# Optimization experiments

Measured on AMD Instinct MI355X. Metric: run time of the kernel, lower is better.

## Reference

```python
import jax, jax.numpy as jnp
import numpy as np

NG, NC = 4096, 4096
FIN_G, FIN_C, D = 512, 512, 256
ALPHA = 0.2
NEG = -9.0e15

def leaky(x):
    return jnp.where(x >= 0, x, ALPHA * x)

def setup_inputs() -> dict:
    key = jax.random.key(0)
    ks = jax.random.split(key, 16)
    gene_x = jax.random.normal(ks[0], (NG, FIN_G), jnp.float32)
    cell_x = jax.random.normal(ks[1], (NC, FIN_C), jnp.float32)
    gene_adj = (jax.random.uniform(ks[2], (NG, NG)) < 0.05).astype(jnp.float32)
    gene_adj = jnp.maximum(gene_adj, jnp.eye(NG, dtype=jnp.float32))
    cell_adj = (jax.random.uniform(ks[3], (NC, NC)) < 0.05).astype(jnp.float32)
    cell_adj = jnp.maximum(cell_adj, jnp.eye(NC, dtype=jnp.float32))
    gene_cell_adj = (jax.random.uniform(ks[4], (NG, NC)) < 0.05).astype(jnp.float32)
    s = 1.414 * np.sqrt(6.0)
    def xav(k, shape):
        lim = s / np.sqrt(shape[0] + shape[1])
        return jax.random.uniform(k, shape, jnp.float32, -lim, lim)
    Wg = xav(ks[5], (D, FIN_G))
    Wc = xav(ks[6], (D, FIN_C))
    a_gg = xav(ks[7], (2 * D, 1))
    a_gc = xav(ks[8], (2 * D, 1))
    a_cc = xav(ks[9], (2 * D, 1))
    a_cg = xav(ks[10], (2 * D, 1))
    gate_g_w = xav(ks[11], (1, D))
    gate_c_w = xav(ks[12], (1, D))
    gate_g_b = jnp.full((1,), -2.0, jnp.float32)
    gate_c_b = jnp.full((1,), -2.0, jnp.float32)
    return dict(gene_x=gene_x, cell_x=cell_x, gene_adj=gene_adj, cell_adj=cell_adj,
                gene_cell_adj=gene_cell_adj, Wg=Wg, Wc=Wc, a_gg=a_gg, a_gc=a_gc,
                a_cc=a_cc, a_cg=a_cg, gate_g_w=gate_g_w, gate_g_b=gate_g_b,
                gate_c_w=gate_c_w, gate_c_b=gate_c_b)

def _gat_block(src_h, dst_h, a, adj):
    # attention of src rows over dst columns; adj: [Ns, Nd]
    d = src_h.shape[1]
    s1 = src_h @ a[:d, :]          # [Ns,1]
    s2 = dst_h @ a[d:, :]          # [Nd,1]
    e = leaky(s1 + s2.T)           # [Ns,Nd]
    att = jax.nn.softmax(jnp.where(adj > 0, e, NEG), axis=1)
    return att @ dst_h             # [Ns,d]

def reference(gene_x, cell_x, gene_adj, cell_adj, gene_cell_adj,
              Wg, Wc, a_gg, a_gc, a_cc, a_cg,
              gate_g_w, gate_g_b, gate_c_w, gate_c_b):
    gene_h = gene_x @ Wg.T   # [Ng,D]
    cell_h = cell_x @ Wc.T   # [Nc,D]
    gene_from_gene = _gat_block(gene_h, gene_h, a_gg, gene_adj)
    gene_from_cell = _gat_block(gene_h, cell_h, a_gc, gene_cell_adj)
    cell_from_cell = _gat_block(cell_h, cell_h, a_cc, cell_adj)
    cell_from_gene = _gat_block(cell_h, gene_h, a_cg, gene_cell_adj.T)
    gamma_g = jax.nn.sigmoid(gene_h @ gate_g_w.T + gate_g_b)  # [Ng,1]
    gamma_c = jax.nn.sigmoid(cell_h @ gate_c_w.T + gate_c_b)  # [Nc,1]
    gene_out = leaky(gene_h + gene_from_gene + gamma_g * gene_from_cell)
    cell_out = leaky(cell_h + cell_from_cell + gamma_c * cell_from_gene)
    return gene_out, cell_out
```

## Files before the change

### kernel.cpp

```cpp
#include <hip/hip_runtime.h>
#include <stdint.h>

#define NGC 4096
#define FIN 512
#define DD  256

typedef __attribute__((ext_vector_type(8))) short short8;
typedef __attribute__((ext_vector_type(4))) float f32x4;
typedef unsigned short u16;
typedef unsigned int   u32;
typedef unsigned long long u64;

static __device__ __forceinline__ float bf2f(u16 u){ return __uint_as_float(((u32)u)<<16); }
static __device__ __forceinline__ u16 f2bf(float f){
  u32 u = __float_as_uint(f);
  u += 0x7fffu + ((u>>16)&1u);
  return (u16)(u>>16);
}
static __device__ __forceinline__ u64 pack4bf(f32x4 v){
  u64 r;
  r  = (u64)f2bf(v[0]);
  r |= (u64)f2bf(v[1]) << 16;
  r |= (u64)f2bf(v[2]) << 32;
  r |= (u64)f2bf(v[3]) << 48;
  return r;
}
static __device__ __forceinline__ float lk(float x){ return fmaxf(x, 0.2f*x); }
static __device__ __forceinline__ u64 shfl_xor64(u64 x, int m){
  u32 lo = (u32)x, hi = (u32)(x >> 32);
  lo = __shfl_xor(lo, m); hi = __shfl_xor(hi, m);
  return ((u64)hi << 32) | lo;
}
static __device__ __forceinline__ u64 spread4(u64 x){
  x &= 0xFFFFull;
  x = (x | (x << 24)) & 0x000000FF000000FFull;
  x = (x | (x << 12)) & 0x000F000F000F000Full;
  x = (x | (x << 6))  & 0x0303030303030303ull;
  x = (x | (x << 3))  & 0x1111111111111111ull;
  return x;
}
static __device__ __forceinline__ void gl16(const void* g, void* l){
  __builtin_amdgcn_global_load_lds(
    (const __attribute__((address_space(1))) void*)g,
    (__attribute__((address_space(3))) void*)l, 16, 0, 0);
}

__global__ __launch_bounds__(512) void k_front(
    const float* __restrict__ gene_adj, const float* __restrict__ cell_adj,
    const float* __restrict__ gc_adj,   u64* __restrict__ packbits,
    const float* __restrict__ xg, const float* __restrict__ xc,
    const float* __restrict__ Wgf, const float* __restrict__ Wcf,
    float* __restrict__ hg, float* __restrict__ hc,
    u16* __restrict__ hTg, u16* __restrict__ hTc)
{
  __shared__ __align__(16) char smem[32768];
  const int t = threadIdx.x;
  const int wid = t >> 6, lane = t & 63;

  if(blockIdx.x < 256){
    int w = blockIdx.x*8 + wid;
    int row0 = w*6;
    const int sel = lane >> 2;
    const int sh = (lane & 3) * 16;

    float4 bufA[16], bufB[16];
    {
      int m = row0 >> 12;
      const float* sp = (m==0) ? gene_adj : (m==1) ? cell_adj : gc_adj;
      const float* rp = sp + (size_t)(row0 & 4095)*NGC + lane*4;
      #pragma unroll
      for(int j=0;j<16;j++) bufA[j] = *(const float4*)(rp + j*256);
    }
    #pragma unroll
    for(int i=0;i<6;i++){
      const bool evn = (i & 1) == 0;
      if(i < 5){
        int row = row0 + i + 1;
        int m = row >> 12;
        const float* sp = (m==0) ? gene_adj : (m==1) ? cell_adj : gc_adj;
        const float* rp = sp + (size_t)(row & 4095)*NGC + lane*4;
        if(evn){
          #pragma unroll
          for(int j=0;j<16;j++) bufB[j] = *(const float4*)(rp + j*256);
        } else {
          #pragma unroll
          for(int j=0;j<16;j++) bufA[j] = *(const float4*)(rp + j*256);
        }
      }
      u64 k0=0, k1=0, k2=0, k3=0;
      #pragma unroll
      for(int j=0;j<16;j++){
        float4 v = evn ? bufA[j] : bufB[j];
        u64 b0 = __ballot(v.x != 0.0f);
        u64 b1 = __ballot(v.y != 0.0f);
        u64 b2 = __ballot(v.z != 0.0f);
        u64 b3 = __ballot(v.w != 0.0f);
        if(sel == j){ k0=b0; k1=b1; k2=b2; k3=b3; }
      }
      u64 wv = spread4(k0 >> sh) | (spread4(k1 >> sh) << 1)
             | (spread4(k2 >> sh) << 2) | (spread4(k3 >> sh) << 3);
      int row = row0 + i;
      packbits[((size_t)(row >> 12) << 18) + (size_t)(row & 4095)*64 + lane] = wv;
    }
    return;
  }

  const int bid = blockIdx.x - 256;
  const int side = bid >> 6;
  const float* x = side ? xc : xg;
  const float* Wf = side ? Wcf : Wgf;
  float* h  = side ? hc : hg;
  u16*  hT  = side ? hTc : hTg;
  const int r0 = (bid & 63) * 64;
  const int lrow = lane & 15, lhi = lane >> 4;

  f32x4 acc[4][2];
  const f32x4 z4 = {0.f,0.f,0.f,0.f};
  #pragma unroll
  for(int i=0;i<4;i++){ acc[i][0]=z4; acc[i][1]=z4; }

  const int r = t >> 3, c8 = t & 7;
  for(int k0 = 0; k0 < FIN; k0 += 64){
    const float* xp = x + (size_t)(r0 + r)*FIN + k0 + c8*8;
    float4 xa = *(const float4*)xp;
    float4 xb = *(const float4*)(xp + 4);
    short8 xv;
    xv[0]=(short)f2bf(xa.x); xv[1]=(short)f2bf(xa.y);
    xv[2]=(short)f2bf(xa.z); xv[3]=(short)f2bf(xa.w);
    xv[4]=(short)f2bf(xb.x); xv[5]=(short)f2bf(xb.y);
    xv[6]=(short)f2bf(xb.z); xv[7]=(short)f2bf(xb.w);
    int wbyte = r*128 + (((c8 ^ (r & 7)) & 7) << 4);
    *(short8*)(smem + wbyte) = xv;
    __syncthreads();
    #pragma unroll
    for(int ksub = 0; ksub < 2; ksub++){
      short8 b[2];
      #pragma unroll
      for(int nf=0; nf<2; nf++){
        int n = wid*32 + nf*16 + lrow;
        const float* wp = Wf + (size_t)n*FIN + k0 + ksub*32 + lhi*8;
        float4 wa = *(const float4*)wp;
        float4 wb = *(const float4*)(wp + 4);
        short8 bb;
        bb[0]=(short)f2bf(wa.x); bb[1]=(short)f2bf(wa.y);
        bb[2]=(short)f2bf(wa.z); bb[3]=(short)f2bf(wa.w);
        bb[4]=(short)f2bf(wb.x); bb[5]=(short)f2bf(wb.y);
        bb[6]=(short)f2bf(wb.z); bb[7]=(short)f2bf(wb.w);
        b[nf] = bb;
      }
      #pragma unroll
      for(int mf=0; mf<4; mf++){
        int row = mf*16 + lrow;
        int g = ksub*4 + lhi;
        short8 a = *(const short8*)(smem + row*128 + (((g ^ (row & 7)) & 7) << 4));
        #pragma unroll
        for(int nf=0; nf<2; nf++)
          acc[mf][nf] = __builtin_amdgcn_mfma_f32_16x16x32_bf16(a, b[nf], acc[mf][nf], 0,0,0);
      }
    }
    __syncthreads();
  }
  #pragma unroll
  for(int mf=0; mf<4; mf++){
    #pragma unroll
    for(int nf=0; nf<2; nf++){
      int col = wid*32 + nf*16 + lrow;
      #pragma unroll
      for(int j=0;j<4;j++){
        int row = mf*16 + lhi*4 + j;
        float v = acc[mf][nf][j];
        h[(size_t)(r0+row)*DD + col] = v;
        int byte_ = col*128 + (((row*2) ^ ((col & 7)<<4)));
        *(u16*)(smem + byte_) = f2bf(v);
      }
    }
  }
  __syncthreads();
  {
    int n = t >> 1, half = t & 1;
    #pragma unroll
    for(int gi=0; gi<4; gi++){
      int g = half*4 + gi;
      int byte_ = n*128 + (((g ^ (n & 7)) & 7) << 4);
      short8 v = *(const short8*)(smem + byte_);
      int kcol = r0 + g*8;
      size_t off = (size_t)(kcol>>5)*8192 + (size_t)(n>>4)*512
                 + ((kcol>>3)&3)*128 + (n&15)*8;
      *(short8*)(hT + off) = v;
    }
  }
}

__global__ __launch_bounds__(256) void k_bitTT(
    const u64* __restrict__ gcb, u64* __restrict__ bT)
{
  int t = threadIdx.x, wid = t>>6, lane = t&63;
  int id = blockIdx.x*4 + wid;
  int G = id & 63, C = id >> 6;

  u64 x = gcb[(size_t)(64*G + lane)*64 + C];

  const u64 M1  = 0xAAAAAAAAAAAAAAAAull;
  const u64 M2  = 0xCCCCCCCCCCCCCCCCull;
  const u64 M4  = 0xF0F0F0F0F0F0F0F0ull;
  const u64 M8  = 0xFF00FF00FF00FF00ull;
  const u64 M16 = 0xFFFF0000FFFF0000ull;
  const u64 M32 = 0xFFFFFFFF00000000ull;
  #define TSTEP(S, M) { u64 y = shfl_xor64(x, S); \
    x = (lane & S) ? ((x & (M)) | ((y >> S) & ~(M))) \
                   : ((x & ~(M)) | ((y << S) & (M))); }
  TSTEP(32, M32) TSTEP(16, M16) TSTEP(8, M8)
  TSTEP(4,  M4)  TSTEP(2,  M2)  TSTEP(1, M1)
  #undef TSTEP

  bT[(size_t)(64*C + lane)*64 + G] = x;
}

__global__ __launch_bounds__(256) void k_svec(
    const float* __restrict__ hg, const float* __restrict__ hc,
    const float* __restrict__ a_gg, const float* __restrict__ a_gc,
    const float* __restrict__ a_cc, const float* __restrict__ a_cg,
    const float* __restrict__ gw_g, const float* __restrict__ gb_g,
    const float* __restrict__ gw_c, const float* __restrict__ gb_c,
    float* __restrict__ sbuf)
{
  int t = threadIdx.x, wid = t>>6, lane = t&63;
  int idx = blockIdx.x * 4 + wid;
  int side = idx >> 12;
  int row  = idx & 4095;
  const float* h = (side ? hc : hg) + (size_t)row*DD;
  const float* v0 = (side ? a_cc : a_gg);
  const float* v1 = (side ? a_cc : a_gg) + DD;
  const float* v2 = (side ? a_cg : a_gc);
  const float* v3 = (side ? a_gc : a_cg) + DD;
  const float* gw = side ? gw_c : gw_g;
  float bias = (side ? gb_c : gb_g)[0];

  float4 hv = *(const float4*)(h + lane*4);
  float4 w0 = *(const float4*)(v0 + lane*4);
  float4 w1 = *(const float4*)(v1 + lane*4);
  float4 w2 = *(const float4*)(v2 + lane*4);
  float4 w3 = *(const float4*)(v3 + lane*4);
  float4 w4 = *(const float4*)(gw + lane*4);

  float d0 = hv.x*w0.x + hv.y*w0.y + hv.z*w0.z + hv.w*w0.w;
  float d1 = hv.x*w1.x + hv.y*w1.y + hv.z*w1.z + hv.w*w1.w;
  float d2 = hv.x*w2.x + hv.y*w2.y + hv.z*w2.z + hv.w*w2.w;
  float d3 = hv.x*w3.x + hv.y*w3.y + hv.z*w3.z + hv.w*w3.w;
  float d4 = hv.x*w4.x + hv.y*w4.y + hv.z*w4.z + hv.w*w4.w;
  #pragma unroll
  for(int s=1;s<64;s<<=1){
    d0 += __shfl_xor(d0, s); d1 += __shfl_xor(d1, s); d2 += __shfl_xor(d2, s);
    d3 += __shfl_xor(d3, s); d4 += __shfl_xor(d4, s);
  }
  if(lane == 0){
    float gam = 1.f/(1.f + __expf(-(d4 + bias)));
    if(side == 0){
      sbuf[0*4096+row]=d0; sbuf[1*4096+row]=d1; sbuf[2*4096+row]=d2;
      sbuf[3*4096+row]=d3; sbuf[4*4096+row]=gam;
    } else {
      sbuf[5*4096+row]=d0; sbuf[6*4096+row]=d1; sbuf[8*4096+row]=d2;
      sbuf[7*4096+row]=d3; sbuf[9*4096+row]=gam;
    }
  }
}

__global__ __launch_bounds__(256,2) void k_gat(
    const float* __restrict__ sbuf,
    const uint8_t* __restrict__ packbits, const uint8_t* __restrict__ bitsT,
    const u16* __restrict__ hTg, const u16* __restrict__ hTc,
    u16* __restrict__ part, float* __restrict__ Zpart)
{
  const int mode = blockIdx.z;
  const int kc   = blockIdx.y;
  const int nodebase = blockIdx.x * 64;
  const int kcbase   = kc * 2048;

  const float* s1; const float* s2; const uint8_t* bits; const u16* hT;
  if(mode == 0){ s1 = sbuf;        s2 = sbuf+4096;   bits = packbits;           hT = hTg; }
  else if(mode == 1){ s1 = sbuf+2*4096; s2 = sbuf+7*4096; bits = packbits+4194304; hT = hTc; }
  else if(mode == 2){ s1 = sbuf+5*4096; s2 = sbuf+6*4096; bits = packbits+2097152; hT = hTc; }
  else { s1 = sbuf+8*4096; s2 = sbuf+3*4096; bits = bitsT; hT = hTg; }

  const int t = threadIdx.x, wid = t>>6, lane = t&63, lrow = lane&15, lhi = lane>>4;
  const int kh = wid >> 1;
  const int ng_sub = wid & 1;

  __shared__ __align__(16) char U[81920];
  char* A_lds  = U;
  char* mask_l = U + 65536;

  {
    int row = t>>2, seg = t&3;
    const char* g = (const char*)bits + (size_t)(nodebase+row)*512 + kc*256 + seg*64;
    char* drow_ = mask_l + row*256;
    #pragma unroll
    for(int i=0;i<4;i++){
      int slot = seg*4 + i;
      *(ulonglong2*)(drow_ + (((slot ^ (row&7)))<<4)) = *(const ulonglong2*)(g + i*16);
    }
  }
  const char* hTb = (const char*)hT;
  {
    const char* g = hTb + ((size_t)kc*64 + kh*32 + 0)*16384 + ng_sub*8192 + lane*16;
    char* l = A_lds + 0*32768 + kh*16384 + ng_sub*8192;
    #pragma unroll
    for(int i=0;i<8;i++) gl16(g + i*1024, l + i*1024);
  }
  float mxv = -1e30f;
  #pragma unroll
  for(int i=0;i<16;i++){
    float4 v = *(const float4*)(s2 + lane*64 + i*4);
    mxv = fmaxf(mxv, fmaxf(fmaxf(v.x,v.y), fmaxf(v.z,v.w)));
  }
  #pragma unroll
  for(int sh=1; sh<64; sh<<=1) mxv = fmaxf(mxv, __shfl_xor(mxv, sh));
  const float maxs2 = mxv;

  const int wnode = nodebase + ng_sub*32;
  const float L2E = 1.4426950408889634f;
  float c1[2], c2[2], z[2];
  #pragma unroll
  for(int nf=0; nf<2; nf++){
    float s1v = s1[wnode + nf*16 + lrow];
    float m = lk(s1v + maxs2);
    c1[nf] = (s1v - m)*L2E;
    c2[nf] = (0.2f*s1v - m)*L2E;
    z[nf] = 0.f;
  }

  f32x4 acc[16][2];
  const f32x4 zz = {0.f,0.f,0.f,0.f};
  #pragma unroll
  for(int i=0;i<16;i++){ acc[i][0]=zz; acc[i][1]=zz; }

  const float* s2g = s2 + kcbase + kh*1024 + lhi*8;
  const char* mrow0 = mask_l + (ng_sub*32 + lrow)*256;
  const char* mrow1 = mask_l + (ng_sub*32 + 16 + lrow)*256;
  const int mx0 = (ng_sub*32 + lrow) & 7, mx1 = (ng_sub*32 + 16 + lrow) & 7;

  float4 csA = *(const float4*)(s2g);
  float4 csB = *(const float4*)(s2g + 4);

  __syncthreads();

  #pragma unroll 1
  for(int s=0; s<32; s++){
    const int cur = s & 1;
    if(s < 31){
      const char* g = hTb + ((size_t)kc*64 + kh*32 + s + 1)*16384 + ng_sub*8192 + lane*16;
      char* l = A_lds + (cur^1)*32768 + kh*16384 + ng_sub*8192;
      #pragma unroll
      for(int i=0;i<8;i++) gl16(g + i*1024, l + i*1024);
    }
    float4 sA = csA, sB = csB;
    if(s < 31){
      csA = *(const float4*)(s2g + (s+1)*32);
      csB = *(const float4*)(s2g + (s+1)*32 + 4);
    }
    float e1[8], e2[8];
    {
      float sv[8] = {sA.x,sA.y,sA.z,sA.w,sB.x,sB.y,sB.z,sB.w};
      #pragma unroll
      for(int j=0;j<8;j++){ e1[j] = sv[j]*L2E; e2[j] = sv[j]*(0.2f*L2E); }
    }
    const int slot = kh*8 + (s>>2), win = (s&3)*4;
    u32 mw0 = *(const u32*)(mrow0 + ((slot ^ mx0)<<4) + win);
    u32 mw1 = *(const u32*)(mrow1 + ((slot ^ mx1)<<4) + win);
    short8 b[2];
    #pragma unroll
    for(int nf=0; nf<2; nf++){
      u32 mw = nf ? mw1 : mw0;
      u32 w4[4];
      #pragma unroll
      for(int pr=0; pr<4; pr++){
        float bit0 = (float)((mw >> (lhi*8 + 2*pr  )) & 1u);
        float bit1 = (float)((mw >> (lhi*8 + 2*pr+1)) & 1u);
        float p0 = __builtin_amdgcn_exp2f(fmaxf(c1[nf]+e1[2*pr  ], c2[nf]+e2[2*pr  ])) * bit0;
        float p1 = __builtin_amdgcn_exp2f(fmaxf(c1[nf]+e1[2*pr+1], c2[nf]+e2[2*pr+1])) * bit1;
        z[nf] += p0 + p1;
        u32 q0 = __float_as_uint(p0) + 0x8000u;
        u32 q1 = __float_as_uint(p1) + 0x8000u;
        w4[pr] = (q1 & 0xFFFF0000u) | (q0 >> 16);
      }
      union{ u32 u[4]; short8 s8; } cv;
      cv.u[0]=w4[0]; cv.u[1]=w4[1]; cv.u[2]=w4[2]; cv.u[3]=w4[3];
      b[nf] = cv.s8;
    }
    const char* Af = A_lds + cur*32768 + kh*16384 + lane*16;
    #pragma unroll
    for(int mf=0; mf<16; mf++){
      short8 a = *(const short8*)(Af + mf*1024);
      acc[mf][0] = __builtin_amdgcn_mfma_f32_16x16x32_bf16(a, b[0], acc[mf][0], 0,0,0);
      acc[mf][1] = __builtin_amdgcn_mfma_f32_16x16x32_bf16(a, b[1], acc[mf][1], 0,0,0);
    }
    __syncthreads();
  }

  #pragma unroll
  for(int nf=0; nf<2; nf++){
    z[nf] += __shfl_xor(z[nf], 16);
    z[nf] += __shfl_xor(z[nf], 32);
  }
  if(lhi == 0){
    float* zp = Zpart + (size_t)(mode*4 + kc*2 + kh)*4096 + wnode;
    zp[lrow]      = z[0];
    zp[16 + lrow] = z[1];
  }

  __syncthreads();
  float* R = (float*)A_lds;
  u16* po = part + ((size_t)(mode*2 + kc) << 20);
  #pragma unroll
  for(int half=0; half<2; half++){
    if(kh == 1){
      #pragma unroll
      for(int mf8=0; mf8<8; mf8++){
        #pragma unroll
        for(int nf=0; nf<2; nf++){
          int r = ng_sub*32 + nf*16 + lrow;
          int byte_ = r*512 + ((mf8*64 + lhi*16) ^ ((r&7)<<4));
          *(f32x4*)((char*)R + byte_) = acc[half*8 + mf8][nf];
        }
      }
    }
    __syncthreads();
    if(kh == 0){
      #pragma unroll
      for(int mf8=0; mf8<8; mf8++){
        #pragma unroll
        for(int nf=0; nf<2; nf++){
          int r = ng_sub*32 + nf*16 + lrow;
          int byte_ = r*512 + ((mf8*64 + lhi*16) ^ ((r&7)<<4));
          f32x4 o = *(const f32x4*)((const char*)R + byte_);
          o = o + acc[half*8 + mf8][nf];
          int node = nodebase + r;
          *(u64*)(po + (size_t)node*256 + (half*8+mf8)*16 + lhi*4) = pack4bf(o);
        }
      }
    }
    __syncthreads();
  }
}

__global__ __launch_bounds__(256) void k_epi(
    const float* __restrict__ hg, const float* __restrict__ hc,
    const u16* __restrict__ part, const float* __restrict__ Zpart,
    const float* __restrict__ sbuf, float* __restrict__ out)
{
  int idx = blockIdx.x*256 + threadIdx.x;
  int fid = idx*4;
  int side = fid >> 20;
  int l = fid & 1048575;
  int node = l >> 8;
  int modeA = side ? 2 : 0, modeB = side ? 3 : 1;
  const float* h = side ? hc : hg;
  float gam = sbuf[(side ? 9 : 4)*4096 + node];
  float za = Zpart[(size_t)(modeA*4+0)*4096 + node] + Zpart[(size_t)(modeA*4+1)*4096 + node]
           + Zpart[(size_t)(modeA*4+2)*4096 + node] + Zpart[(size_t)(modeA*4+3)*4096 + node];
  float zb = Zpart[(size_t)(modeB*4+0)*4096 + node] + Zpart[(size_t)(modeB*4+1)*4096 + node]
           + Zpart[(size_t)(modeB*4+2)*4096 + node] + Zpart[(size_t)(modeB*4+3)*4096 + node];
  float rza = 1.f / fmaxf(za, 1e-30f);
  float rzb = 1.f / fmaxf(zb, 1e-30f);
  ushort4 a0 = *(const ushort4*)(part + ((size_t)(modeA*2  )<<20) + l);
  ushort4 a1 = *(const ushort4*)(part + ((size_t)(modeA*2+1)<<20) + l);
  ushort4 b0 = *(const ushort4*)(part + ((size_t)(modeB*2  )<<20) + l);
  ushort4 b1 = *(const ushort4*)(part + ((size_t)(modeB*2+1)<<20) + l);
  float4 h4 = *(const float4*)(h + l);
  float4 o;
  o.x = lk(h4.x + (bf2f(a0.x)+bf2f(a1.x))*rza + gam*(bf2f(b0.x)+bf2f(b1.x))*rzb);
  o.y = lk(h4.y + (bf2f(a0.y)+bf2f(a1.y))*rza + gam*(bf2f(b0.y)+bf2f(b1.y))*rzb);
  o.z = lk(h4.z + (bf2f(a0.z)+bf2f(a1.z))*rza + gam*(bf2f(b0.z)+bf2f(b1.z))*rzb);
  o.w = lk(h4.w + (bf2f(a0.w)+bf2f(a1.w))*rza + gam*(bf2f(b0.w)+bf2f(b1.w))*rzb);
  *(float4*)(out + fid) = o;
}

extern "C" void kernel_launch(void* const* d_in, const int* in_sizes, int n_in,
                              void* d_out, int out_size, void* d_ws, size_t ws_size,
                              hipStream_t stream)
{
  const float* gene_x   = (const float*)d_in[0];
  const float* cell_x   = (const float*)d_in[1];
  const float* gene_adj = (const float*)d_in[2];
  const float* cell_adj = (const float*)d_in[3];
  const float* gc_adj   = (const float*)d_in[4];
  const float* Wg       = (const float*)d_in[5];
  const float* Wc       = (const float*)d_in[6];
  const float* a_gg     = (const float*)d_in[7];
  const float* a_gc     = (const float*)d_in[8];
  const float* a_cc     = (const float*)d_in[9];
  const float* a_cg     = (const float*)d_in[10];
  const float* gw_g     = (const float*)d_in[11];
  const float* gb_g     = (const float*)d_in[12];
  const float* gw_c     = (const float*)d_in[13];
  const float* gb_c     = (const float*)d_in[14];

  char* ws = (char*)d_ws;
  float* hg   = (float*)(ws);
  float* hc   = (float*)(ws + (4u<<20));
  u16*   hTg  = (u16*)  (ws + (8u<<20));
  u16*   hTc  = (u16*)  (ws + (10u<<20));
  float* sbuf = (float*)(ws + (12u<<20));
  float* Zpart= (float*)(ws + (12u<<20) + (512u<<10));
  uint8_t* bitsT = (uint8_t*)(ws + (13u<<20));
  u16*   part = (u16*)  (ws + (17u<<20));
  u64*   packbits = (u64*)(ws + (49u<<20));

  k_front<<<dim3(384), 512, 0, stream>>>(gene_adj, cell_adj, gc_adj, packbits,
                                         gene_x, cell_x, Wg, Wc,
                                         hg, hc, hTg, hTc);
  k_bitTT<<<dim3(1024), 256, 0, stream>>>(packbits + 524288, (u64*)bitsT);
  k_svec<<<dim3(2048), 256, 0, stream>>>(hg, hc, a_gg, a_gc, a_cc, a_cg,
                                         gw_g, gb_g, gw_c, gb_c, sbuf);
  k_gat<<<dim3(64,2,4), 256, 0, stream>>>(sbuf, (const uint8_t*)packbits,
                                          bitsT, hTg, hTc, part, Zpart);
  k_epi<<<dim3(2048), 256, 0, stream>>>(hg, hc, part, Zpart, sbuf, (float*)d_out);
}
```

Before: 132.9 us.

## Co-schedule bit packing and projection GEMM across warps of one front kernel

The front kernel used to give adjacency bit-packing and the feature projection GEMM to separate blocks. Now every block runs 6 bit-packing wavefronts of 8 rows each and 2 GEMM wavefronts, so both workloads are interleaved on each CU. Each GEMM wavefront computes a 16-row by 256-column tile straight from global memory with no LDS staging and no block barriers. It writes the transposed bf16 copy directly as packed 4-element stores. This aims to overlap the memory-bound adjacency scan with MFMA work and remove the synchronisation. In exchange, W is reloaded and converted redundantly by every GEMM wave, and stores become less coalesced.

```diff
diff --git a/kernel.cpp b/kernel.cpp
--- a/kernel.cpp
+++ b/kernel.cpp
@@ -25,6 +25,14 @@
   r |= (u64)f2bf(v[3]) << 48;
   return r;
 }
+static __device__ __forceinline__ short8 cvt8(float4 a, float4 b){
+  short8 r;
+  r[0]=(short)f2bf(a.x); r[1]=(short)f2bf(a.y);
+  r[2]=(short)f2bf(a.z); r[3]=(short)f2bf(a.w);
+  r[4]=(short)f2bf(b.x); r[5]=(short)f2bf(b.y);
+  r[6]=(short)f2bf(b.z); r[7]=(short)f2bf(b.w);
+  return r;
+}
 static __device__ __forceinline__ float lk(float x){ return fmaxf(x, 0.2f*x); }
 static __device__ __forceinline__ u64 shfl_xor64(u64 x, int m){
   u32 lo = (u32)x, hi = (u32)(x >> 32);
@@ -53,13 +61,12 @@
     float* __restrict__ hg, float* __restrict__ hc,
     u16* __restrict__ hTg, u16* __restrict__ hTc)
 {
-  __shared__ __align__(16) char smem[32768];
   const int t = threadIdx.x;
   const int wid = t >> 6, lane = t & 63;
 
-  if(blockIdx.x < 256){
-    int w = blockIdx.x*8 + wid;
-    int row0 = w*6;
+  if(wid < 6){
+    int w = blockIdx.x*6 + wid;
+    int row0 = w*8;
     const int sel = lane >> 2;
     const int sh = (lane & 3) * 16;
 
@@ -72,9 +79,9 @@
       for(int j=0;j<16;j++) bufA[j] = *(const float4*)(rp + j*256);
     }
     #pragma unroll
-    for(int i=0;i<6;i++){
+    for(int i=0;i<8;i++){
       const bool evn = (i & 1) == 0;
-      if(i < 5){
+      if(i < 7){
         int row = row0 + i + 1;
         int m = row >> 12;
         const float* sp = (m==0) ? gene_adj : (m==1) ? cell_adj : gc_adj;
@@ -105,89 +112,48 @@
     return;
   }
 
-  const int bid = blockIdx.x - 256;
-  const int side = bid >> 6;
-  const float* x = side ? xc : xg;
+  const int hw = blockIdx.x*2 + (wid - 6);
+  const int side = hw >> 8;
+  const float* x  = side ? xc : xg;
   const float* Wf = side ? Wcf : Wgf;
   float* h  = side ? hc : hg;
   u16*  hT  = side ? hTc : hTg;
-  const int r0 = (bid & 63) * 64;
+  const int r0w = (hw & 255) * 16;
   const int lrow = lane & 15, lhi = lane >> 4;
 
-  f32x4 acc[4][2];
+  f32x4 acc[16];
   const f32x4 z4 = {0.f,0.f,0.f,0.f};
   #pragma unroll
-  for(int i=0;i<4;i++){ acc[i][0]=z4; acc[i][1]=z4; }
-
-  const int r = t >> 3, c8 = t & 7;
-  for(int k0 = 0; k0 < FIN; k0 += 64){
-    const float* xp = x + (size_t)(r0 + r)*FIN + k0 + c8*8;
-    float4 xa = *(const float4*)xp;
-    float4 xb = *(const float4*)(xp + 4);
-    short8 xv;
-    xv[0]=(short)f2bf(xa.x); xv[1]=(short)f2bf(xa.y);
-    xv[2]=(short)f2bf(xa.z); xv[3]=(short)f2bf(xa.w);
-    xv[4]=(short)f2bf(xb.x); xv[5]=(short)f2bf(xb.y);
-    xv[6]=(short)f2bf(xb.z); xv[7]=(short)f2bf(xb.w);
-    int wbyte = r*128 + (((c8 ^ (r & 7)) & 7) << 4);
-    *(short8*)(smem + wbyte) = xv;
-    __syncthreads();
-    #pragma unroll
-    for(int ksub = 0; ksub < 2; ksub++){
-      short8 b[2];
-      #pragma unroll
-      for(int nf=0; nf<2; nf++){
-        int n = wid*32 + nf*16 + lrow;
-        const float* wp = Wf + (size_t)n*FIN + k0 + ksub*32 + lhi*8;
-        float4 wa = *(const float4*)wp;
-        float4 wb = *(const float4*)(wp + 4);
-        short8 bb;
-        bb[0]=(short)f2bf(wa.x); bb[1]=(short)f2bf(wa.y);
-        bb[2]=(short)f2bf(wa.z); bb[3]=(short)f2bf(wa.w);
-        bb[4]=(short)f2bf(wb.x); bb[5]=(short)f2bf(wb.y);
-        bb[6]=(short)f2bf(wb.z); bb[7]=(short)f2bf(wb.w);
-        b[nf] = bb;
-      }
-      #pragma unroll
-      for(int mf=0; mf<4; mf++){
-        int row = mf*16 + lrow;
-        int g = ksub*4 + lhi;
-        short8 a = *(const short8*)(smem + row*128 + (((g ^ (row & 7)) & 7) << 4));
-        #pragma unroll
-        for(int nf=0; nf<2; nf++)
-          acc[mf][nf] = __builtin_amdgcn_mfma_f32_16x16x32_bf16(a, b[nf], acc[mf][nf], 0,0,0);
-      }
-    }
-    __syncthreads();
-  }
-  #pragma unroll
-  for(int mf=0; mf<4; mf++){
-    #pragma unroll
-    for(int nf=0; nf<2; nf++){
-      int col = wid*32 + nf*16 + lrow;
-      #pragma unroll
-      for(int j=0;j<4;j++){
-        int row = mf*16 + lhi*4 + j;
-        float v = acc[mf][nf][j];
-        h[(size_t)(r0+row)*DD + col] = v;
-        int byte_ = col*128 + (((row*2) ^ ((col & 7)<<4)));
-        *(u16*)(smem + byte_) = f2bf(v);
-      }
-    }
-  }
-  __syncthreads();
-  {
-    int n = t >> 1, half = t & 1;
-    #pragma unroll
-    for(int gi=0; gi<4; gi++){
-      int g = half*4 + gi;
-      int byte_ = n*128 + (((g ^ (n & 7)) & 7) << 4);
-      short8 v = *(const short8*)(smem + byte_);
-      int kcol = r0 + g*8;
-      size_t off = (size_t)(kcol>>5)*8192 + (size_t)(n>>4)*512
-                 + ((kcol>>3)&3)*128 + (n&15)*8;
-      *(short8*)(hT + off) = v;
-    }
+  for(int i=0;i<16;i++) acc[i] = z4;
+
+  const float* ap_base = x + (size_t)(r0w + lrow)*FIN + lhi*8;
+  const float* wp_base = Wf + (size_t)lrow*FIN + lhi*8;
+
+  for(int ks = 0; ks < 16; ks++){
+    const int k0 = ks*32;
+    float4 a0 = *(const float4*)(ap_base + k0);
+    float4 a1 = *(const float4*)(ap_base + k0 + 4);
+    short8 af = cvt8(a0, a1);
+    #pragma unroll
+    for(int nf=0; nf<16; nf++){
+      const float* wp = wp_base + (size_t)(nf*16)*FIN + k0;
+      float4 w0 = *(const float4*)wp;
+      float4 w1 = *(const float4*)(wp + 4);
+      short8 bf = cvt8(w0, w1);
+      acc[nf] = __builtin_amdgcn_mfma_f32_16x16x32_bf16(af, bf, acc[nf], 0,0,0);
+    }
+  }
+
+  const int kbase = r0w + 4*lhi;
+  #pragma unroll
+  for(int nf=0; nf<16; nf++){
+    int d = nf*16 + lrow;
+    #pragma unroll
+    for(int j=0;j<4;j++)
+      h[(size_t)(kbase + j)*DD + d] = acc[nf][j];
+    size_t off = (size_t)(kbase>>5)*8192 + (size_t)(d>>4)*512
+               + ((kbase>>3)&3)*128 + (d&15)*8 + (kbase&7);
+    *(u64*)(hT + off) = pack4bf(acc[nf]);
   }
 }
 
@@ -506,7 +472,7 @@
   u16*   part = (u16*)  (ws + (17u<<20));
   u64*   packbits = (u64*)(ws + (49u<<20));
 
-  k_front<<<dim3(384), 512, 0, stream>>>(gene_adj, cell_adj, gc_adj, packbits,
+  k_front<<<dim3(256), 512, 0, stream>>>(gene_adj, cell_adj, gc_adj, packbits,
                                          gene_x, cell_x, Wg, Wc,
                                          hg, hc, hTg, hTc);
   k_bitTT<<<dim3(1024), 256, 0, stream>>>(packbits + 524288, (u64*)bitsT);
```

New measurement: 206.9 us. +55.7%, slower.
